# Kernel optimization log

Measured on AMD Instinct MI355X. Metric: run time of the kernel, lower is better.

The kernel has to match this reference:

```python
import jax, jax.numpy as jnp
import numpy as np

EMB = 1024
HEADS = 16
DH = EMB // HEADS
EPS = 1e-5


def setup_inputs() -> dict:
    key = jax.random.key(0)
    ks = jax.random.split(key, 8)
    s = 0.02
    return {
        "x": jax.random.normal(ks[0], (4, 2048, EMB), dtype=jnp.float32),
        "Wq": jax.random.normal(ks[1], (EMB, EMB), dtype=jnp.float32) * s,
        "Wk": jax.random.normal(ks[2], (EMB, EMB), dtype=jnp.float32) * s,
        "Wv": jax.random.normal(ks[3], (EMB, EMB), dtype=jnp.float32) * s,
        "Wo": jax.random.normal(ks[4], (EMB, EMB), dtype=jnp.float32) * s,
        "bo": jnp.zeros((EMB,), dtype=jnp.float32),
        "W1": jax.random.normal(ks[5], (EMB, 4 * EMB), dtype=jnp.float32) * s,
        "b1": jnp.zeros((4 * EMB,), dtype=jnp.float32),
        "W2": jax.random.normal(ks[6], (4 * EMB, EMB), dtype=jnp.float32) * s,
        "b2": jnp.zeros((EMB,), dtype=jnp.float32),
        "g1": jnp.ones((EMB,), dtype=jnp.float32),
        "beta1": jnp.zeros((EMB,), dtype=jnp.float32),
        "g2": jnp.ones((EMB,), dtype=jnp.float32),
        "beta2": jnp.zeros((EMB,), dtype=jnp.float32),
    }


def _layernorm(x, scale, bias):
    mean = jnp.mean(x, axis=-1, keepdims=True)
    var = jnp.mean((x - mean) ** 2, axis=-1, keepdims=True)  # unbiased=False
    return scale * ((x - mean) / jnp.sqrt(var + EPS)) + bias


def _attention(x, Wq, Wk, Wv, Wo, bo):
    B, S, _ = x.shape
    q = (x @ Wq).reshape(B, S, HEADS, DH).transpose(0, 2, 1, 3)  # b h s d
    k = (x @ Wk).reshape(B, S, HEADS, DH).transpose(0, 2, 1, 3)
    v = (x @ Wv).reshape(B, S, HEADS, DH).transpose(0, 2, 1, 3)
    scores = jnp.einsum("bhqd,bhkd->bhqk", q, k)
    causal = jnp.tril(jnp.ones((S, S), dtype=bool))
    scores = jnp.where(causal, scores, -jnp.inf)
    w = jax.nn.softmax(scores / jnp.sqrt(jnp.float32(DH)), axis=-1)
    ctx = jnp.einsum("bhqk,bhkd->bhqd", w, v).transpose(0, 2, 1, 3).reshape(B, S, HEADS * DH)
    return ctx @ Wo + bo


def reference(x, Wq, Wk, Wv, Wo, bo, W1, b1, W2, b2, g1, beta1, g2, beta2):
    # pre-LN attention + residual
    h = x + _attention(_layernorm(x, g1, beta1), Wq, Wk, Wv, Wo, bo)
    # pre-LN FFN (exact GELU, as torch nn.GELU default) + residual
    y = _layernorm(h, g2, beta2)
    y = jax.nn.gelu(y @ W1 + b1, approximate=False) @ W2 + b2
    return h + y
```

## Files before the change

kernel.cpp:

```cpp
#include <hip/hip_runtime.h>
#include <hip/hip_bf16.h>

#define EMB 1024
#define SEQ 2048
#define BATCH 4
#define TOK (BATCH*SEQ)
#define NH 16
#define DH 64
#define FF 4096

typedef unsigned short u16;
typedef __bf16 bf16x8 __attribute__((ext_vector_type(8)));
typedef float f32x4 __attribute__((ext_vector_type(4)));

union frag_u { uint4 u4; bf16x8 bf; u16 us[8]; };

__device__ __forceinline__ u16 f2bf(float f) {
  union { float f; unsigned u; } a; a.f = f;
  unsigned r = a.u + 0x7fffu + ((a.u >> 16) & 1u);
  return (u16)(r >> 16);
}

__device__ __forceinline__ void glds16(const void* g, void* l) {
  __builtin_amdgcn_global_load_lds((const __attribute__((address_space(1))) void*)g,
                                   (__attribute__((address_space(3))) void*)l, 16, 0, 0);
}

__device__ __forceinline__ float gelu_fast(float u) {
  float u2 = u * u;
  float c = fmaf(u2, 0.0356774081f, 0.7978845608f);
  float e = __expf(2.f * u * c);
  return u * e * __builtin_amdgcn_rcpf(e + 1.f);
}

__global__ __launch_bounds__(256) void cvt_t_kernel(const float* __restrict__ src,
                                                    u16* __restrict__ dst,
                                                    int N, int ldk) {
  __shared__ float tile[32][33];
  int c0 = blockIdx.x * 32, r0 = blockIdx.y * 32;
  int tc = threadIdx.x & 31, tr = threadIdx.x >> 5;
  #pragma unroll
  for (int p = 0; p < 4; p++)
    tile[tr + p * 8][tc] = src[(size_t)(r0 + tr + p * 8) * N + c0 + tc];
  __syncthreads();
  #pragma unroll
  for (int p = 0; p < 4; p++)
    dst[(size_t)(c0 + tr + p * 8) * ldk + r0 + tc] = f2bf(tile[tc][tr + p * 8]);
}

__global__ __launch_bounds__(256) void ln_kernel(const float* __restrict__ x,
                                                 const float* __restrict__ g,
                                                 const float* __restrict__ be,
                                                 u16* __restrict__ out) {
  int wave = threadIdx.x >> 6, lane = threadIdx.x & 63;
  int row = blockIdx.x * 4 + wave;
  const float* xr = x + (size_t)row * EMB;
  float4 v[4];
  float s = 0.f;
  #pragma unroll
  for (int i = 0; i < 4; i++) {
    v[i] = *(const float4*)(xr + i * 256 + lane * 4);
    s += v[i].x + v[i].y + v[i].z + v[i].w;
  }
  #pragma unroll
  for (int m = 1; m < 64; m <<= 1) s += __shfl_xor(s, m, 64);
  float mean = s * (1.f / EMB);
  float vs = 0.f;
  #pragma unroll
  for (int i = 0; i < 4; i++) {
    float dx;
    dx = v[i].x - mean; vs += dx * dx;
    dx = v[i].y - mean; vs += dx * dx;
    dx = v[i].z - mean; vs += dx * dx;
    dx = v[i].w - mean; vs += dx * dx;
  }
  #pragma unroll
  for (int m = 1; m < 64; m <<= 1) vs += __shfl_xor(vs, m, 64);
  float inv = rsqrtf(vs * (1.f / EMB) + 1e-5f);
  u16* orow = out + (size_t)row * EMB;
  #pragma unroll
  for (int i = 0; i < 4; i++) {
    int c = i * 256 + lane * 4;
    float4 gv = *(const float4*)(g + c);
    float4 bv = *(const float4*)(be + c);
    ushort4 o;
    o.x = f2bf(gv.x * (v[i].x - mean) * inv + bv.x);
    o.y = f2bf(gv.y * (v[i].y - mean) * inv + bv.y);
    o.z = f2bf(gv.z * (v[i].z - mean) * inv + bv.z);
    o.w = f2bf(gv.w * (v[i].w - mean) * inv + bv.w);
    *(ushort4*)(orow + c) = o;
  }
}

template <int MODE>
__global__ __launch_bounds__(256) void gemm128(const u16* __restrict__ A,
                                               const u16* __restrict__ Bt,
                                               const float* __restrict__ bias,
                                               const float* __restrict__ resid,
                                               void* __restrict__ outp,
                                               int N, int K) {
  __shared__ __align__(16) u16 As[128 * 64];
  __shared__ __align__(16) u16 Bs[128 * 64];
  const int t = threadIdx.x;
  const int w = t >> 6, lane = t & 63;
  const int l15 = lane & 15, quad = lane >> 4;
  const int wr = w >> 1, wc = w & 1;
  const int rowBase = blockIdx.y * 128, colBase = blockIdx.x * 128;

  const int sr = lane >> 3;
  const int sc = ((lane & 7) ^ sr) * 8;
  const u16* gA = A + (size_t)(rowBase + w * 8 + sr) * K + sc;
  const u16* gB = Bt + (size_t)(colBase + w * 8 + sr) * K + sc;
  u16* lA = As + w * 8 * 64;
  u16* lB = Bs + w * 8 * 64;

  const int swz0 = (quad ^ (l15 & 7)) * 8;
  const int swz1 = ((quad + 4) ^ (l15 & 7)) * 8;

  f32x4 zero = {0.f, 0.f, 0.f, 0.f};
  f32x4 acc[4][4];
  #pragma unroll
  for (int i = 0; i < 4; i++)
    #pragma unroll
    for (int j = 0; j < 4; j++) acc[i][j] = zero;

  for (int k0 = 0; k0 < K; k0 += 64) {
    __syncthreads();
    #pragma unroll
    for (int j = 0; j < 4; j++) {
      glds16(gA + (size_t)(j * 32) * K + k0, lA + j * 32 * 64);
      glds16(gB + (size_t)(j * 32) * K + k0, lB + j * 32 * 64);
    }
    __syncthreads();
    #pragma unroll
    for (int kk = 0; kk < 2; kk++) {
      const int so = kk ? swz1 : swz0;
      frag_u a4[4], b4[4];
      #pragma unroll
      for (int mi = 0; mi < 4; mi++)
        a4[mi].u4 = *(const uint4*)(As + (wr * 64 + mi * 16 + l15) * 64 + so);
      #pragma unroll
      for (int ni = 0; ni < 4; ni++)
        b4[ni].u4 = *(const uint4*)(Bs + (wc * 64 + ni * 16 + l15) * 64 + so);
      #pragma unroll
      for (int mi = 0; mi < 4; mi++)
        #pragma unroll
        for (int ni = 0; ni < 4; ni++)
          acc[mi][ni] = __builtin_amdgcn_mfma_f32_16x16x32_bf16(a4[mi].bf, b4[ni].bf, acc[mi][ni], 0, 0, 0);
    }
  }

  #pragma unroll
  for (int mi = 0; mi < 4; mi++) {
    #pragma unroll
    for (int ni = 0; ni < 4; ni++) {
      int col = colBase + wc * 64 + ni * 16 + l15;
      int row0 = rowBase + wr * 64 + mi * 16 + quad * 4;
      if (MODE == 1) {
        int mat = col >> 10, cc = col & 1023;
        int hh = cc >> 6, d = cc & 63;
        int b = row0 >> 11, s0 = row0 & 2047;
        if (mat == 2) {
          uint2 pk;
          pk.x = (unsigned)f2bf(acc[mi][ni][0]) | ((unsigned)f2bf(acc[mi][ni][1]) << 16);
          pk.y = (unsigned)f2bf(acc[mi][ni][2]) | ((unsigned)f2bf(acc[mi][ni][3]) << 16);
          *(uint2*)((u16*)outp + 2 * (size_t)TOK * EMB +
                    ((size_t)((b * NH + hh) * DH + d)) * SEQ + s0) = pk;
        } else {
          #pragma unroll
          for (int r = 0; r < 4; r++)
            ((u16*)outp)[(size_t)mat * (TOK * EMB) +
                         (((size_t)(b * NH + hh) * SEQ + s0 + r) << 6) + d] = f2bf(acc[mi][ni][r]);
        }
      } else {
        #pragma unroll
        for (int r = 0; r < 4; r++) {
          int row = row0 + r;
          float vv = acc[mi][ni][r];
          if (MODE == 2) {
            vv = gelu_fast(vv + bias[col]);
            ((u16*)outp)[(size_t)row * N + col] = f2bf(vv);
          } else {
            vv += bias[col] + resid[(size_t)row * N + col];
            ((float*)outp)[(size_t)row * N + col] = vv;
          }
        }
      }
    }
  }
}

__global__ __launch_bounds__(256) void attn_kernel(const u16* __restrict__ q,
                                                   const u16* __restrict__ k,
                                                   const u16* __restrict__ vt,
                                                   u16* __restrict__ ctx) {
  __shared__ __align__(16) u16 Ks[64 * 72];
  __shared__ __align__(16) u16 Vs[64 * 72];
  __shared__ __align__(16) u16 Ps[128 * 72];
  __shared__ float Ls[128];
  const int t = threadIdx.x;
  const int w = t >> 6, lane = t & 63;
  const int l15 = lane & 15, quad = lane >> 4;
  const int bh = blockIdx.x, pr_ = blockIdx.y;
  const size_t base = (size_t)bh * SEQ * DH;
  const int bq = bh >> 4, hh = bh & 15;

  const int sr = t >> 2, scol = (t & 3) * 8;
  const u16* gK = k + base + (size_t)sr * DH + scol;
  const u16* gV = vt + base + (size_t)sr * SEQ + scol;
  u16* sK = Ks + sr * 72 + scol;
  u16* sV = Vs + sr * 72 + scol;

  f32x4 zero = {0.f, 0.f, 0.f, 0.f};
  uint4 rK0, rK1, rV0, rV1;
  rK0 = *(const uint4*)(gK);
  rK1 = *(const uint4*)(gK + 32);
  rV0 = *(const uint4*)(gV);
  rV1 = *(const uint4*)(gV + 32);

  for (int ti = 0; ti < 2; ti++) {
    const int qt = ti ? (15 - pr_) : pr_;
    const int qBase = qt * 128;
    const int ktEnd = 2 * qt + 1;

    frag_u qf[2][2];
    #pragma unroll
    for (int ni = 0; ni < 2; ni++)
      #pragma unroll
      for (int ks = 0; ks < 2; ks++)
        qf[ni][ks].u4 = *(const uint4*)(q + base +
            (size_t)(qBase + w * 32 + ni * 16 + l15) * DH + ks * 32 + quad * 8);

    f32x4 oacc[2][4];
    #pragma unroll
    for (int mi = 0; mi < 2; mi++)
      #pragma unroll
      for (int n0 = 0; n0 < 4; n0++) oacc[mi][n0] = zero;
    float l0 = 0.f, l1 = 0.f;

    for (int kt = 0; kt <= ktEnd; kt++) {
      __syncthreads();
      *(uint4*)sK = rK0; *(uint4*)(sK + 32) = rK1;
      *(uint4*)sV = rV0; *(uint4*)(sV + 32) = rV1;
      __syncthreads();
      int nkt = (kt < ktEnd) ? kt + 1 : (ti == 0 ? 0 : -1);
      if (nkt >= 0) {
        rK0 = *(const uint4*)(gK + (size_t)(nkt * 64) * DH);
        rK1 = *(const uint4*)(gK + (size_t)(nkt * 64) * DH + 32);
        rV0 = *(const uint4*)(gV + nkt * 64);
        rV1 = *(const uint4*)(gV + nkt * 64 + 32);
      }
      const int rel = kt - 2 * qt;
      if (rel == 1 && w < 2) continue;

      frag_u kf[4][2];
      #pragma unroll
      for (int mi = 0; mi < 4; mi++)
        #pragma unroll
        for (int ks = 0; ks < 2; ks++)
          kf[mi][ks].u4 = *(const uint4*)(Ks + (mi * 16 + l15) * 72 + ks * 32 + quad * 8);
      f32x4 st[4][2];
      #pragma unroll
      for (int mi = 0; mi < 4; mi++)
        #pragma unroll
        for (int ni = 0; ni < 2; ni++) st[mi][ni] = zero;
      #pragma unroll
      for (int ks = 0; ks < 2; ks++)
        #pragma unroll
        for (int mi = 0; mi < 4; mi++)
          #pragma unroll
          for (int ni = 0; ni < 2; ni++)
            st[mi][ni] = __builtin_amdgcn_mfma_f32_16x16x32_bf16(kf[mi][ks].bf, qf[ni][ks].bf, st[mi][ni], 0, 0, 0);

      const bool doMask = (rel == 0 && w < 2) || (rel == 1);
      #pragma unroll
      for (int ni = 0; ni < 2; ni++) {
        const int qrow = qBase + w * 32 + ni * 16 + l15;
        float sum = 0.f;
        u16* prow = Ps + (w * 32 + ni * 16 + l15) * 72;
        #pragma unroll
        for (int mi = 0; mi < 4; mi++) {
          float p[4];
          #pragma unroll
          for (int r = 0; r < 4; r++) {
            p[r] = __expf(st[mi][ni][r] * 0.125f);
            if (doMask && (kt * 64 + mi * 16 + quad * 4 + r) > qrow) p[r] = 0.f;
            sum += p[r];
          }
          uint2 pk;
          pk.x = (unsigned)f2bf(p[0]) | ((unsigned)f2bf(p[1]) << 16);
          pk.y = (unsigned)f2bf(p[2]) | ((unsigned)f2bf(p[3]) << 16);
          *(uint2*)(prow + mi * 16 + quad * 4) = pk;
        }
        sum += __shfl_xor(sum, 16, 64);
        sum += __shfl_xor(sum, 32, 64);
        if (ni == 0) l0 += sum; else l1 += sum;
      }

      frag_u pa[2][2];
      #pragma unroll
      for (int mi = 0; mi < 2; mi++)
        #pragma unroll
        for (int ks = 0; ks < 2; ks++)
          pa[mi][ks].u4 = *(const uint4*)(Ps + (w * 32 + mi * 16 + l15) * 72 + ks * 32 + quad * 8);
      #pragma unroll
      for (int ks = 0; ks < 2; ks++)
        #pragma unroll
        for (int n0 = 0; n0 < 4; n0++) {
          frag_u b;
          b.u4 = *(const uint4*)(Vs + (n0 * 16 + l15) * 72 + ks * 32 + quad * 8);
          #pragma unroll
          for (int mi = 0; mi < 2; mi++)
            oacc[mi][n0] = __builtin_amdgcn_mfma_f32_16x16x32_bf16(pa[mi][ks].bf, b.bf, oacc[mi][n0], 0, 0, 0);
        }
    }

    if (quad == 0) {
      Ls[w * 32 + l15] = l0;
      Ls[w * 32 + 16 + l15] = l1;
    }
    #pragma unroll
    for (int mi = 0; mi < 2; mi++) {
      float il[4];
      #pragma unroll
      for (int r = 0; r < 4; r++) il[r] = 1.f / Ls[w * 32 + mi * 16 + quad * 4 + r];
      #pragma unroll
      for (int n0 = 0; n0 < 4; n0++) {
        int s = qBase + w * 32 + mi * 16 + quad * 4;
        int col = hh * 64 + n0 * 16 + l15;
        #pragma unroll
        for (int r = 0; r < 4; r++)
          ctx[((size_t)(bq * SEQ + s + r)) * EMB + col] = f2bf(oacc[mi][n0][r] * il[r]);
      }
    }
  }
}

extern "C" void kernel_launch(void* const* d_in, const int* in_sizes, int n_in,
                              void* d_out, int out_size, void* d_ws, size_t ws_size,
                              hipStream_t stream) {
  const float* x  = (const float*)d_in[0];
  const float* Wq = (const float*)d_in[1];
  const float* Wk = (const float*)d_in[2];
  const float* Wv = (const float*)d_in[3];
  const float* Wo = (const float*)d_in[4];
  const float* bo = (const float*)d_in[5];
  const float* W1 = (const float*)d_in[6];
  const float* b1 = (const float*)d_in[7];
  const float* W2 = (const float*)d_in[8];
  const float* b2 = (const float*)d_in[9];
  const float* g1  = (const float*)d_in[10];
  const float* be1 = (const float*)d_in[11];
  const float* g2  = (const float*)d_in[12];
  const float* be2 = (const float*)d_in[13];
  float* out = (float*)d_out;
  char* ws = (char*)d_ws;
  const size_t MB = 1u << 20;

  u16* wqkv_t = (u16*)(ws + 0 * MB);
  u16* wo_t   = (u16*)(ws + 6 * MB);
  u16* w1_t   = (u16*)(ws + 8 * MB);
  u16* w2_t   = (u16*)(ws + 16 * MB);
  float* hbuf = (float*)(ws + 24 * MB);
  u16* r1 = (u16*)(ws + 56 * MB);
  u16* qb = (u16*)(ws + 72 * MB);
  u16* f1 = (u16*)(ws + 72 * MB);

  cvt_t_kernel<<<dim3(32, 32), 256, 0, stream>>>(Wq, wqkv_t, 1024, 1024);
  cvt_t_kernel<<<dim3(32, 32), 256, 0, stream>>>(Wk, wqkv_t + 1024 * 1024, 1024, 1024);
  cvt_t_kernel<<<dim3(32, 32), 256, 0, stream>>>(Wv, wqkv_t + 2 * 1024 * 1024, 1024, 1024);
  cvt_t_kernel<<<dim3(32, 32), 256, 0, stream>>>(Wo, wo_t, 1024, 1024);
  cvt_t_kernel<<<dim3(128, 32), 256, 0, stream>>>(W1, w1_t, 4096, 1024);
  cvt_t_kernel<<<dim3(32, 128), 256, 0, stream>>>(W2, w2_t, 1024, 4096);

  ln_kernel<<<2048, 256, 0, stream>>>(x, g1, be1, r1);

  gemm128<1><<<dim3(24, 64), 256, 0, stream>>>(r1, wqkv_t, nullptr, nullptr, qb, 3072, 1024);

  attn_kernel<<<dim3(64, 8), 256, 0, stream>>>(qb, qb + (size_t)TOK * EMB,
                                               qb + 2 * (size_t)TOK * EMB, r1);

  gemm128<3><<<dim3(8, 64), 256, 0, stream>>>(r1, wo_t, bo, x, hbuf, 1024, 1024);

  ln_kernel<<<2048, 256, 0, stream>>>(hbuf, g2, be2, r1);

  gemm128<2><<<dim3(32, 64), 256, 0, stream>>>(r1, w1_t, b1, nullptr, f1, 4096, 1024);

  gemm128<3><<<dim3(8, 64), 256, 0, stream>>>(f1, w2_t, b2, hbuf, out, 1024, 4096);
}
```

Before: 529.9 us.

## Merge weight conversions, store residual in bf16, add 256-row GEMM tiles

Merges the six weight-transpose launches into a single prep kernel. Stores the intermediate residual h as bf16 instead of fp32, and adds a bf16-input layernorm variant to read it. Adds a 512-thread gemm256 kernel with 256x128 tiles for the QKV and FFN1 projections to raise B-tile reuse. These cut launch overhead and memory traffic, but rounding h to bf16 lowers the precision of both residual paths, and the larger tiles mean fewer blocks in flight.

After: 504.2 us. -4.8%, faster.

```diff
diff --git a/kernel.cpp b/kernel.cpp
--- a/kernel.cpp
+++ b/kernel.cpp
@@ -20,6 +20,9 @@
   unsigned r = a.u + 0x7fffu + ((a.u >> 16) & 1u);
   return (u16)(r >> 16);
 }
+__device__ __forceinline__ float bf2f(u16 u) {
+  union { unsigned u; float f; } a; a.u = ((unsigned)u) << 16; return a.f;
+}
 
 __device__ __forceinline__ void glds16(const void* g, void* l) {
   __builtin_amdgcn_global_load_lds((const __attribute__((address_space(1))) void*)g,
@@ -33,11 +36,11 @@
   return u * e * __builtin_amdgcn_rcpf(e + 1.f);
 }
 
-__global__ __launch_bounds__(256) void cvt_t_kernel(const float* __restrict__ src,
-                                                    u16* __restrict__ dst,
-                                                    int N, int ldk) {
+__device__ __forceinline__ void cvt_t_body(const float* __restrict__ src,
+                                           u16* __restrict__ dst,
+                                           int N, int ldk, int bx, int by) {
   __shared__ float tile[32][33];
-  int c0 = blockIdx.x * 32, r0 = blockIdx.y * 32;
+  int c0 = bx * 32, r0 = by * 32;
   int tc = threadIdx.x & 31, tr = threadIdx.x >> 5;
   #pragma unroll
   for (int p = 0; p < 4; p++)
@@ -48,32 +51,60 @@
     dst[(size_t)(c0 + tr + p * 8) * ldk + r0 + tc] = f2bf(tile[tc][tr + p * 8]);
 }
 
-__global__ __launch_bounds__(256) void ln_kernel(const float* __restrict__ x,
+__global__ __launch_bounds__(256) void prep_kernel(const float* Wq, const float* Wk,
+                                                   const float* Wv, const float* Wo,
+                                                   const float* W1, const float* W2,
+                                                   u16* wqkv_t, u16* wo_t,
+                                                   u16* w1_t, u16* w2_t) {
+  int id = blockIdx.x;
+  if (id < 4096) {
+    const float* s = (id < 1024) ? Wq : (id < 2048) ? Wk : (id < 3072) ? Wv : Wo;
+    u16* d = (id < 1024) ? wqkv_t : (id < 2048) ? wqkv_t + 1024 * 1024
+           : (id < 3072) ? wqkv_t + 2 * 1024 * 1024 : wo_t;
+    int local = id & 1023;
+    cvt_t_body(s, d, 1024, 1024, local & 31, local >> 5);
+  } else if (id < 8192) {
+    int local = id - 4096;
+    cvt_t_body(W1, w1_t, 4096, 1024, local & 127, local >> 7);
+  } else {
+    int local = id - 8192;
+    cvt_t_body(W2, w2_t, 1024, 4096, local & 31, local >> 5);
+  }
+}
+
+template <int IN_BF16>
+__global__ __launch_bounds__(256) void ln_kernel(const void* __restrict__ xv,
                                                  const float* __restrict__ g,
                                                  const float* __restrict__ be,
                                                  u16* __restrict__ out) {
   int wave = threadIdx.x >> 6, lane = threadIdx.x & 63;
   int row = blockIdx.x * 4 + wave;
-  const float* xr = x + (size_t)row * EMB;
-  float4 v[4];
+  float v[16];
   float s = 0.f;
-  #pragma unroll
-  for (int i = 0; i < 4; i++) {
-    v[i] = *(const float4*)(xr + i * 256 + lane * 4);
-    s += v[i].x + v[i].y + v[i].z + v[i].w;
+  if (IN_BF16) {
+    const u16* xr = (const u16*)xv + (size_t)row * EMB;
+    #pragma unroll
+    for (int i = 0; i < 4; i++) {
+      ushort4 u = *(const ushort4*)(xr + i * 256 + lane * 4);
+      v[i * 4 + 0] = bf2f(u.x); v[i * 4 + 1] = bf2f(u.y);
+      v[i * 4 + 2] = bf2f(u.z); v[i * 4 + 3] = bf2f(u.w);
+      s += v[i * 4] + v[i * 4 + 1] + v[i * 4 + 2] + v[i * 4 + 3];
+    }
+  } else {
+    const float* xr = (const float*)xv + (size_t)row * EMB;
+    #pragma unroll
+    for (int i = 0; i < 4; i++) {
+      float4 u = *(const float4*)(xr + i * 256 + lane * 4);
+      v[i * 4 + 0] = u.x; v[i * 4 + 1] = u.y; v[i * 4 + 2] = u.z; v[i * 4 + 3] = u.w;
+      s += u.x + u.y + u.z + u.w;
+    }
   }
   #pragma unroll
   for (int m = 1; m < 64; m <<= 1) s += __shfl_xor(s, m, 64);
   float mean = s * (1.f / EMB);
   float vs = 0.f;
   #pragma unroll
-  for (int i = 0; i < 4; i++) {
-    float dx;
-    dx = v[i].x - mean; vs += dx * dx;
-    dx = v[i].y - mean; vs += dx * dx;
-    dx = v[i].z - mean; vs += dx * dx;
-    dx = v[i].w - mean; vs += dx * dx;
-  }
+  for (int i = 0; i < 16; i++) { float dx = v[i] - mean; vs += dx * dx; }
   #pragma unroll
   for (int m = 1; m < 64; m <<= 1) vs += __shfl_xor(vs, m, 64);
   float inv = rsqrtf(vs * (1.f / EMB) + 1e-5f);
@@ -84,28 +115,27 @@
     float4 gv = *(const float4*)(g + c);
     float4 bv = *(const float4*)(be + c);
     ushort4 o;
-    o.x = f2bf(gv.x * (v[i].x - mean) * inv + bv.x);
-    o.y = f2bf(gv.y * (v[i].y - mean) * inv + bv.y);
-    o.z = f2bf(gv.z * (v[i].z - mean) * inv + bv.z);
-    o.w = f2bf(gv.w * (v[i].w - mean) * inv + bv.w);
+    o.x = f2bf(gv.x * (v[i * 4 + 0] - mean) * inv + bv.x);
+    o.y = f2bf(gv.y * (v[i * 4 + 1] - mean) * inv + bv.y);
+    o.z = f2bf(gv.z * (v[i * 4 + 2] - mean) * inv + bv.z);
+    o.w = f2bf(gv.w * (v[i * 4 + 3] - mean) * inv + bv.w);
     *(ushort4*)(orow + c) = o;
   }
 }
 
 template <int MODE>
-__global__ __launch_bounds__(256) void gemm128(const u16* __restrict__ A,
+__global__ __launch_bounds__(512) void gemm256(const u16* __restrict__ A,
                                                const u16* __restrict__ Bt,
                                                const float* __restrict__ bias,
-                                               const float* __restrict__ resid,
                                                void* __restrict__ outp,
                                                int N, int K) {
-  __shared__ __align__(16) u16 As[128 * 64];
+  __shared__ __align__(16) u16 As[256 * 64];
   __shared__ __align__(16) u16 Bs[128 * 64];
   const int t = threadIdx.x;
   const int w = t >> 6, lane = t & 63;
   const int l15 = lane & 15, quad = lane >> 4;
   const int wr = w >> 1, wc = w & 1;
-  const int rowBase = blockIdx.y * 128, colBase = blockIdx.x * 128;
+  const int rowBase = blockIdx.y * 256, colBase = blockIdx.x * 128;
 
   const int sr = lane >> 3;
   const int sc = ((lane & 7) ^ sr) * 8;
@@ -127,10 +157,11 @@
   for (int k0 = 0; k0 < K; k0 += 64) {
     __syncthreads();
     #pragma unroll
-    for (int j = 0; j < 4; j++) {
-      glds16(gA + (size_t)(j * 32) * K + k0, lA + j * 32 * 64);
-      glds16(gB + (size_t)(j * 32) * K + k0, lB + j * 32 * 64);
-    }
+    for (int j = 0; j < 4; j++)
+      glds16(gA + (size_t)(j * 64) * K + k0, lA + j * 64 * 64);
+    #pragma unroll
+    for (int j = 0; j < 2; j++)
+      glds16(gB + (size_t)(j * 64) * K + k0, lB + j * 64 * 64);
     __syncthreads();
     #pragma unroll
     for (int kk = 0; kk < 2; kk++) {
@@ -175,15 +206,88 @@
       } else {
         #pragma unroll
         for (int r = 0; r < 4; r++) {
-          int row = row0 + r;
-          float vv = acc[mi][ni][r];
-          if (MODE == 2) {
-            vv = gelu_fast(vv + bias[col]);
-            ((u16*)outp)[(size_t)row * N + col] = f2bf(vv);
-          } else {
-            vv += bias[col] + resid[(size_t)row * N + col];
-            ((float*)outp)[(size_t)row * N + col] = vv;
-          }
+          float vv = gelu_fast(acc[mi][ni][r] + bias[col]);
+          ((u16*)outp)[(size_t)(row0 + r) * N + col] = f2bf(vv);
+        }
+      }
+    }
+  }
+}
+
+template <int MODE>
+__global__ __launch_bounds__(256) void gemm128(const u16* __restrict__ A,
+                                               const u16* __restrict__ Bt,
+                                               const float* __restrict__ bias,
+                                               const void* __restrict__ resid,
+                                               void* __restrict__ outp,
+                                               int N, int K) {
+  __shared__ __align__(16) u16 As[128 * 64];
+  __shared__ __align__(16) u16 Bs[128 * 64];
+  const int t = threadIdx.x;
+  const int w = t >> 6, lane = t & 63;
+  const int l15 = lane & 15, quad = lane >> 4;
+  const int wr = w >> 1, wc = w & 1;
+  const int rowBase = blockIdx.y * 128, colBase = blockIdx.x * 128;
+
+  const int sr = lane >> 3;
+  const int sc = ((lane & 7) ^ sr) * 8;
+  const u16* gA = A + (size_t)(rowBase + w * 8 + sr) * K + sc;
+  const u16* gB = Bt + (size_t)(colBase + w * 8 + sr) * K + sc;
+  u16* lA = As + w * 8 * 64;
+  u16* lB = Bs + w * 8 * 64;
+
+  const int swz0 = (quad ^ (l15 & 7)) * 8;
+  const int swz1 = ((quad + 4) ^ (l15 & 7)) * 8;
+
+  f32x4 zero = {0.f, 0.f, 0.f, 0.f};
+  f32x4 acc[4][4];
+  #pragma unroll
+  for (int i = 0; i < 4; i++)
+    #pragma unroll
+    for (int j = 0; j < 4; j++) acc[i][j] = zero;
+
+  for (int k0 = 0; k0 < K; k0 += 64) {
+    __syncthreads();
+    #pragma unroll
+    for (int j = 0; j < 4; j++) {
+      glds16(gA + (size_t)(j * 32) * K + k0, lA + j * 32 * 64);
+      glds16(gB + (size_t)(j * 32) * K + k0, lB + j * 32 * 64);
+    }
+    __syncthreads();
+    #pragma unroll
+    for (int kk = 0; kk < 2; kk++) {
+      const int so = kk ? swz1 : swz0;
+      frag_u a4[4], b4[4];
+      #pragma unroll
+      for (int mi = 0; mi < 4; mi++)
+        a4[mi].u4 = *(const uint4*)(As + (wr * 64 + mi * 16 + l15) * 64 + so);
+      #pragma unroll
+      for (int ni = 0; ni < 4; ni++)
+        b4[ni].u4 = *(const uint4*)(Bs + (wc * 64 + ni * 16 + l15) * 64 + so);
+      #pragma unroll
+      for (int mi = 0; mi < 4; mi++)
+        #pragma unroll
+        for (int ni = 0; ni < 4; ni++)
+          acc[mi][ni] = __builtin_amdgcn_mfma_f32_16x16x32_bf16(a4[mi].bf, b4[ni].bf, acc[mi][ni], 0, 0, 0);
+    }
+  }
+
+  #pragma unroll
+  for (int mi = 0; mi < 4; mi++) {
+    #pragma unroll
+    for (int ni = 0; ni < 4; ni++) {
+      int col = colBase + wc * 64 + ni * 16 + l15;
+      int row0 = rowBase + wr * 64 + mi * 16 + quad * 4;
+      #pragma unroll
+      for (int r = 0; r < 4; r++) {
+        int row = row0 + r;
+        float vv = acc[mi][ni][r] + bias[col];
+        if (MODE == 3) {
+          vv += ((const float*)resid)[(size_t)row * N + col];
+          ((u16*)outp)[(size_t)row * N + col] = f2bf(vv);
+        } else {
+          vv += bf2f(((const u16*)resid)[(size_t)row * N + col]);
+          ((float*)outp)[(size_t)row * N + col] = vv;
         }
       }
     }
@@ -361,30 +465,26 @@
   u16* wo_t   = (u16*)(ws + 6 * MB);
   u16* w1_t   = (u16*)(ws + 8 * MB);
   u16* w2_t   = (u16*)(ws + 16 * MB);
-  float* hbuf = (float*)(ws + 24 * MB);
+  u16* hbuf   = (u16*)(ws + 24 * MB);
   u16* r1 = (u16*)(ws + 56 * MB);
   u16* qb = (u16*)(ws + 72 * MB);
   u16* f1 = (u16*)(ws + 72 * MB);
 
-  cvt_t_kernel<<<dim3(32, 32), 256, 0, stream>>>(Wq, wqkv_t, 1024, 1024);
-  cvt_t_kernel<<<dim3(32, 32), 256, 0, stream>>>(Wk, wqkv_t + 1024 * 1024, 1024, 1024);
-  cvt_t_kernel<<<dim3(32, 32), 256, 0, stream>>>(Wv, wqkv_t + 2 * 1024 * 1024, 1024, 1024);
-  cvt_t_kernel<<<dim3(32, 32), 256, 0, stream>>>(Wo, wo_t, 1024, 1024);
-  cvt_t_kernel<<<dim3(128, 32), 256, 0, stream>>>(W1, w1_t, 4096, 1024);
-  cvt_t_kernel<<<dim3(32, 128), 256, 0, stream>>>(W2, w2_t, 1024, 4096);
-
-  ln_kernel<<<2048, 256, 0, stream>>>(x, g1, be1, r1);
-
-  gemm128<1><<<dim3(24, 64), 256, 0, stream>>>(r1, wqkv_t, nullptr, nullptr, qb, 3072, 1024);
+  prep_kernel<<<12288, 256, 0, stream>>>(Wq, Wk, Wv, Wo, W1, W2,
+                                         wqkv_t, wo_t, w1_t, w2_t);
+
+  ln_kernel<0><<<2048, 256, 0, stream>>>(x, g1, be1, r1);
+
+  gemm256<1><<<dim3(24, 32), 512, 0, stream>>>(r1, wqkv_t, nullptr, qb, 3072, 1024);
 
   attn_kernel<<<dim3(64, 8), 256, 0, stream>>>(qb, qb + (size_t)TOK * EMB,
                                                qb + 2 * (size_t)TOK * EMB, r1);
 
   gemm128<3><<<dim3(8, 64), 256, 0, stream>>>(r1, wo_t, bo, x, hbuf, 1024, 1024);
 
-  ln_kernel<<<2048, 256, 0, stream>>>(hbuf, g2, be2, r1);
-
-  gemm128<2><<<dim3(32, 64), 256, 0, stream>>>(r1, w1_t, b1, nullptr, f1, 4096, 1024);
-
-  gemm128<3><<<dim3(8, 64), 256, 0, stream>>>(f1, w2_t, b2, hbuf, out, 1024, 4096);
-}
+  ln_kernel<1><<<2048, 256, 0, stream>>>(hbuf, g2, be2, r1);
+
+  gemm256<2><<<dim3(32, 32), 512, 0, stream>>>(r1, w1_t, b1, f1, 4096, 1024);
+
+  gemm128<4><<<dim3(8, 64), 256, 0, stream>>>(f1, w2_t, b2, hbuf, out, 1024, 4096);
+}
```
